# Optimization experiments

Hardware: AMD Instinct MI355X
Metric: run time of the kernel (lower is better)

Reference implementation:

```python
import jax, jax.numpy as jnp
import numpy as np

N_NODES = 100000
N_EDGES = 1600000
D = 128


def setup_inputs() -> dict:
    key = jax.random.key(0)
    k1, k2, k3, k4, k5 = jax.random.split(key, 5)
    x = jax.random.normal(k1, (N_NODES, D), dtype=jnp.float32)
    edge_index = jax.random.randint(k2, (2, N_EDGES), 0, N_NODES, dtype=jnp.int32)
    edge_weight = jax.random.uniform(k3, (N_EDGES,), dtype=jnp.float32)
    W_lin = jax.random.normal(k4, (D, D), dtype=jnp.float32) / np.sqrt(D)
    W_gcn = jax.random.normal(k5, (D, D), dtype=jnp.float32) / np.sqrt(D)
    return {"x": x, "edge_index": edge_index, "edge_weight": edge_weight,
            "W_lin": W_lin, "W_gcn": W_gcn}


def reference(x, edge_index, edge_weight, W_lin, W_gcn):
    # hl = Linear(x) (no bias)
    hl = x @ W_lin  # [N, D]

    # GCNConv with add_self_loops=False, normalize=True, no bias:
    row = edge_index[0]  # src
    col = edge_index[1]  # dst
    # symmetric gcn_norm from edge weights (degree scattered onto dst)
    deg = jax.ops.segment_sum(edge_weight, col, num_segments=x.shape[0])  # [N]
    deg_inv_sqrt = jnp.where(deg > 0, jax.lax.rsqrt(deg), 0.0)
    norm = deg_inv_sqrt[row] * edge_weight * deg_inv_sqrt[col]  # [E]

    h = x @ W_gcn  # [N, D] transform before propagate
    msg = h[row] * norm[:, None]  # [E, D] gather + scale
    hr = jax.ops.segment_sum(msg, col, num_segments=x.shape[0])  # scatter-add [N, D]

    return hl + hr
```

## Files before the change

kernel.cpp:

```cpp
#include <hip/hip_runtime.h>

#define NN 100000
#define NE 1600000
#define DD 128
#define NB 1563
#define HIST_BLKS 256
#define CAST_BLKS 752
#define WT2_BLKS  16
#define K1_BLKS (HIST_BLKS + CAST_BLKS + WT2_BLKS)
#define BINCAP 1536

typedef __attribute__((ext_vector_type(8))) short bf16x8;
typedef __attribute__((ext_vector_type(4))) float f32x4;

__device__ inline unsigned short f2bf(float f) {
  union { float f; unsigned u; } v; v.f = f;
  unsigned r = (v.u + 0x7FFF + ((v.u >> 16) & 1)) >> 16;
  return (unsigned short)r;
}

__global__ __launch_bounds__(512) void kb1(const int* __restrict__ col,
    const float* __restrict__ x, const float* __restrict__ Wl, const float* __restrict__ Wg,
    unsigned* __restrict__ hist, unsigned short* __restrict__ xb, unsigned short* __restrict__ WT2) {
  __shared__ unsigned h1[NB];
  int b = blockIdx.x, tid = threadIdx.x;
  if (b < HIST_BLKS) {
    for (int i = tid; i < NB; i += 512) h1[i] = 0;
    __syncthreads();
    for (int e = b * 512 + tid; e < NE; e += HIST_BLKS * 512)
      atomicAdd(&h1[((unsigned)col[e]) >> 6], 1u);
    __syncthreads();
    for (int i = tid; i < NB; i += 512) hist[(size_t)i * HIST_BLKS + b] = h1[i];
  } else if (b < HIST_BLKS + CAST_BLKS) {
    int bb = b - HIST_BLKS;
    const int total8 = NN * DD / 8;
    for (int i = bb * 512 + tid; i < total8; i += CAST_BLKS * 512) {
      float4 a = *(const float4*)&x[i * 8];
      float4 q = *(const float4*)&x[i * 8 + 4];
      unsigned short o[8] = {f2bf(a.x), f2bf(a.y), f2bf(a.z), f2bf(a.w),
                             f2bf(q.x), f2bf(q.y), f2bf(q.z), f2bf(q.w)};
      *(uint4*)&xb[i * 8] = *(uint4*)o;
    }
  } else {
    int bb = b - HIST_BLKS - CAST_BLKS;
    int j = bb * 8 + (tid >> 6);
    int l = tid & 63;
    for (int k = l; k < 256; k += 64) {
      const float* W = (k < DD) ? Wl : Wg;
      WT2[j * 256 + k] = f2bf(W[(k & (DD - 1)) * DD + j]);
    }
  }
}

__global__ __launch_bounds__(256) void kb2a(const unsigned* __restrict__ hist,
    unsigned* __restrict__ binTotal) {
  int w = (blockIdx.x * 256 + threadIdx.x) >> 6, l = threadIdx.x & 63;
  if (w >= NB) return;
  unsigned s = 0;
  for (int k = l; k < HIST_BLKS; k += 64) s += hist[(size_t)w * HIST_BLKS + k];
  #pragma unroll
  for (int off = 32; off >= 1; off >>= 1) s += __shfl_down(s, off, 64);
  if (l == 0) binTotal[w] = s;
}

__global__ __launch_bounds__(512) void kb2b(const unsigned* __restrict__ binTotal,
    unsigned* __restrict__ binBase) {
  __shared__ unsigned ps[512];
  int t = threadIdx.x;
  unsigned v[4], s = 0;
  #pragma unroll
  for (int k = 0; k < 4; k++) { int i = t * 4 + k; v[k] = (i < NB) ? binTotal[i] : 0; s += v[k]; }
  ps[t] = s;
  __syncthreads();
  for (int off = 1; off < 512; off <<= 1) {
    unsigned u = (t >= off) ? ps[t - off] : 0;
    __syncthreads();
    ps[t] += u;
    __syncthreads();
  }
  unsigned run = ps[t] - s;
  #pragma unroll
  for (int k = 0; k < 4; k++) { int i = t * 4 + k; if (i < NB + 1) binBase[i] = run; run += v[k]; }
}

__global__ __launch_bounds__(256) void kb2c(const unsigned* __restrict__ hist,
    const unsigned* __restrict__ binBase, unsigned* __restrict__ off) {
  int w = (blockIdx.x * 256 + threadIdx.x) >> 6, l = threadIdx.x & 63;
  if (w >= NB) return;
  unsigned v[4], s = 0;
  #pragma unroll
  for (int k = 0; k < 4; k++) { v[k] = hist[(size_t)w * HIST_BLKS + l * 4 + k]; s += v[k]; }
  unsigned incl = s;
  #pragma unroll
  for (int o = 1; o < 64; o <<= 1) { unsigned tt = __shfl_up(incl, o, 64); if (l >= o) incl += tt; }
  unsigned run = binBase[w] + incl - s;
  #pragma unroll
  for (int k = 0; k < 4; k++) { off[(size_t)(l * 4 + k) * NB + w] = run; run += v[k]; }
}

__global__ __launch_bounds__(512) void kb3(const int* __restrict__ row, const int* __restrict__ col,
    const float* __restrict__ ew, const unsigned* __restrict__ off,
    unsigned long long* __restrict__ entries) {
  __shared__ unsigned cnt[NB];
  int b = blockIdx.x, tid = threadIdx.x;
  for (int i = tid; i < NB; i += 512) cnt[i] = off[(size_t)b * NB + i];
  __syncthreads();
  for (int e = b * 512 + tid; e < NE; e += HIST_BLKS * 512) {
    int c = col[e];
    unsigned pos = atomicAdd(&cnt[((unsigned)c) >> 6], 1u);
    entries[pos] = ((unsigned long long)__float_as_uint(ew[e]) << 32)
                 | ((unsigned)row[e] << 6) | (unsigned)(c & 63);
  }
}

__global__ __launch_bounds__(256) void kb4(const unsigned long long* __restrict__ entries,
    const unsigned* __restrict__ binBase, float* __restrict__ dis) {
  __shared__ unsigned degFx[64];
  int bin = blockIdx.x, tid = threadIdx.x;
  if (tid < 64) degFx[tid] = 0;
  __syncthreads();
  unsigned s0 = binBase[bin], n = binBase[bin + 1] - s0;
  for (unsigned i = tid; i < n; i += 256) {
    unsigned long long e = entries[s0 + i];
    float w = __uint_as_float((unsigned)(e >> 32));
    atomicAdd(&degFx[(unsigned)e & 63], (unsigned)(w * 67108864.0f + 0.5f));
  }
  __syncthreads();
  if (tid < 64) {
    int node = bin * 64 + tid;
    if (node < NN) {
      float d = (float)degFx[tid] * (1.0f / 67108864.0f);
      dis[node] = (d > 0.0f) ? rsqrtf(d) : 0.0f;
    }
  }
}

__global__ __launch_bounds__(512) void kb5(const unsigned long long* __restrict__ entries,
    const unsigned* __restrict__ binBase, const float* __restrict__ dis,
    const unsigned short* __restrict__ xb, unsigned short* __restrict__ yb) {
  __shared__ unsigned long long raw[BINCAP], srt[BINCAP];
  __shared__ unsigned short rnk[BINCAP];
  __shared__ unsigned cnt64[64];
  __shared__ unsigned base64[64];
  int bin = blockIdx.x, tid = threadIdx.x;
  unsigned s0 = binBase[bin];
  int n = (int)(binBase[bin + 1] - s0);
  if (n > BINCAP) n = BINCAP;
  if (tid < 64) cnt64[tid] = 0;
  for (int i = tid; i < n; i += 512) raw[i] = entries[s0 + i];
  __syncthreads();
  for (int i = tid; i < n; i += 512)
    rnk[i] = (unsigned short)atomicAdd(&cnt64[(unsigned)raw[i] & 63], 1u);
  __syncthreads();
  if (tid < 64) {
    unsigned v = cnt64[tid], incl = v;
    #pragma unroll
    for (int o = 1; o < 64; o <<= 1) { unsigned t2 = __shfl_up(incl, o, 64); if (tid >= o) incl += t2; }
    base64[tid] = incl - v;
  }
  __syncthreads();
  for (int i = tid; i < n; i += 512) {
    unsigned long long e = raw[i];
    srt[base64[(unsigned)e & 63] + rnk[i]] = e;
  }
  __syncthreads();
  for (int i = tid; i < n; i += 512) {
    unsigned long long e = srt[i];
    unsigned src = ((unsigned)e) >> 6;
    float wn = __uint_as_float((unsigned)(e >> 32)) * dis[src];
    srt[i] = ((unsigned long long)__float_as_uint(wn) << 32) | (unsigned)(e & 0xFFFFFFFFu);
  }
  __syncthreads();
  int wv = tid >> 6, lane = tid & 63, grp = lane >> 4, l16 = lane & 15;
  for (int dd = 0; dd < 8; ++dd) {
    int d = wv * 8 + dd;
    int c = bin * 64 + d;
    if (c >= NN) break;
    int e0 = base64[d], m = cnt64[d];
    float acc[8] = {};
    for (int i = 0; i < m; i += 8) {
      int ja = i + grp, jb = i + 4 + grp;
      unsigned sa = 0, sb = 0;
      float wa = 0.f, wb = 0.f;
      if (ja < m) { unsigned long long e = srt[e0 + ja]; sa = ((unsigned)e) >> 6; wa = __uint_as_float((unsigned)(e >> 32)); }
      if (jb < m) { unsigned long long e = srt[e0 + jb]; sb = ((unsigned)e) >> 6; wb = __uint_as_float((unsigned)(e >> 32)); }
      uint4 ha = *(const uint4*)&xb[(size_t)sa * DD + l16 * 8];
      uint4 hb = *(const uint4*)&xb[(size_t)sb * DD + l16 * 8];
      union { uint4 v; unsigned u[4]; } qa, qb;
      qa.v = ha; qb.v = hb;
      #pragma unroll
      for (int k = 0; k < 4; k++) {
        union { unsigned u; float f; } lo, hi;
        lo.u = qa.u[k] << 16;
        hi.u = qa.u[k] & 0xFFFF0000u;
        acc[2 * k]     += wa * lo.f;
        acc[2 * k + 1] += wa * hi.f;
        lo.u = qb.u[k] << 16;
        hi.u = qb.u[k] & 0xFFFF0000u;
        acc[2 * k]     += wb * lo.f;
        acc[2 * k + 1] += wb * hi.f;
      }
    }
    #pragma unroll
    for (int k = 0; k < 8; k++) {
      acc[k] += __shfl_xor(acc[k], 16, 64);
      acc[k] += __shfl_xor(acc[k], 32, 64);
    }
    if (grp == 0) {
      float dc = dis[c];
      unsigned short o[8] = {f2bf(acc[0] * dc), f2bf(acc[1] * dc), f2bf(acc[2] * dc),
                             f2bf(acc[3] * dc), f2bf(acc[4] * dc), f2bf(acc[5] * dc),
                             f2bf(acc[6] * dc), f2bf(acc[7] * dc)};
      *(uint4*)&yb[(size_t)c * DD + l16 * 8] = *(uint4*)o;
    }
  }
}

__global__ __launch_bounds__(256) void k_gemm(const unsigned short* __restrict__ xb,
    const unsigned short* __restrict__ yb, const unsigned short* __restrict__ WT2,
    float* __restrict__ out, int N) {
  __shared__ __align__(16) unsigned short Bl[128 * 256];
  __shared__ __align__(16) unsigned short Al[64 * 256];
  int t = threadIdx.x;
  int rowbase = blockIdx.x * 64;

  const uint4* WTv = (const uint4*)WT2;
  #pragma unroll
  for (int i = 0; i < 16; i++) {
    int ci = t + i * 256;
    int j = ci >> 5, c16 = ci & 31;
    uint4 v = WTv[ci];
    int byte = j * 512 + c16 * 16;
    byte ^= (j & 7) << 4;
    *(uint4*)((char*)Bl + byte) = v;
  }
  #pragma unroll
  for (int i = 0; i < 8; i++) {
    int ci = t + i * 256;
    int r = ci >> 5, c16 = ci & 31;
    int gr = rowbase + r;
    uint4 v = make_uint4(0, 0, 0, 0);
    if (gr < N) {
      if (c16 < 16) v = *(const uint4*)&xb[(size_t)gr * DD + c16 * 8];
      else          v = *(const uint4*)&yb[(size_t)gr * DD + (c16 - 16) * 8];
    }
    int byte = r * 512 + c16 * 16;
    byte ^= (r & 7) << 4;
    *(uint4*)((char*)Al + byte) = v;
  }
  __syncthreads();

  int wid = t >> 6, lane = t & 63;
  int wn = wid * 32;
  int l15 = lane & 15, l4 = lane >> 4;
  f32x4 acc[4][2] = {};
  #pragma unroll
  for (int kk = 0; kk < 8; kk++) {
    bf16x8 af[4], bfr[2];
    #pragma unroll
    for (int m = 0; m < 4; m++) {
      int r = m * 16 + l15;
      int byte = r * 512 + kk * 64 + l4 * 16;
      byte ^= (r & 7) << 4;
      af[m] = *(const bf16x8*)((const char*)Al + byte);
    }
    #pragma unroll
    for (int n = 0; n < 2; n++) {
      int r = wn + n * 16 + l15;
      int byte = r * 512 + kk * 64 + l4 * 16;
      byte ^= (r & 7) << 4;
      bfr[n] = *(const bf16x8*)((const char*)Bl + byte);
    }
    #pragma unroll
    for (int m = 0; m < 4; m++)
      #pragma unroll
      for (int n = 0; n < 2; n++)
        acc[m][n] = __builtin_amdgcn_mfma_f32_16x16x32_bf16(af[m], bfr[n], acc[m][n], 0, 0, 0);
  }

  #pragma unroll
  for (int m = 0; m < 4; m++) {
    int gr0 = rowbase + m * 16 + l4 * 4;
    #pragma unroll
    for (int n = 0; n < 2; n++) {
      int gc = wn + n * 16 + l15;
      #pragma unroll
      for (int j = 0; j < 4; j++) {
        int gr = gr0 + j;
        if (gr < N) out[(size_t)gr * DD + gc] = acc[m][n][j];
      }
    }
  }
}

extern "C" void kernel_launch(void* const* d_in, const int* in_sizes, int n_in,
                              void* d_out, int out_size, void* d_ws, size_t ws_size,
                              hipStream_t stream) {
  const float* x  = (const float*)d_in[0];
  const int*   ei = (const int*)d_in[1];
  const float* ew = (const float*)d_in[2];
  const float* Wl = (const float*)d_in[3];
  const float* Wg = (const float*)d_in[4];
  float* out = (float*)d_out;
  const int* row = ei;
  const int* col = ei + NE;

  const size_t MB = 1u << 20;
  char* base = (char*)d_ws;
  unsigned* hist     = (unsigned*)(base);
  unsigned* off      = (unsigned*)(base + 2 * MB);
  unsigned* binTotal = (unsigned*)(base + 4 * MB);
  unsigned* binBase  = (unsigned*)(base + 4 * MB + 32768);
  unsigned long long* entries = (unsigned long long*)(base + 5 * MB);
  float* dis = (float*)(base + 18 * MB);
  unsigned short* xb = (unsigned short*)(base + 19 * MB);
  unsigned short* yb = (unsigned short*)(base + 45 * MB);
  unsigned short* WT2 = (unsigned short*)(base + 71 * MB);

  kb1<<<K1_BLKS, 512, 0, stream>>>(col, x, Wl, Wg, hist, xb, WT2);
  kb2a<<<(NB + 3) / 4, 256, 0, stream>>>(hist, binTotal);
  kb2b<<<1, 512, 0, stream>>>(binTotal, binBase);
  kb2c<<<(NB + 3) / 4, 256, 0, stream>>>(hist, binBase, off);
  kb3<<<HIST_BLKS, 512, 0, stream>>>(row, col, ew, off, entries);
  kb4<<<NB, 256, 0, stream>>>(entries, binBase, dis);
  kb5<<<NB, 512, 0, stream>>>(entries, binBase, dis, xb, yb);
  k_gemm<<<(NN + 63) / 64, 256, 0, stream>>>(xb, yb, WT2, out, NN);
}
```

Baseline: 161.2 us.

## Halve histogram blocks, unroll gather loop 4-way, use nontemporal output stores

Three separate changes. The histogram/scatter stage now uses 128 blocks instead of 256, which shrinks the per-block offset table and the scan work. The aggregation loop now issues four independent bf16 row gathers per iteration instead of two, so more memory loads are in flight. The GEMM output writes use nontemporal stores to avoid polluting cache. Fewer histogram blocks means less parallelism in the scatter kernel, and the deeper unroll raises register pressure.

```diff
diff --git a/kernel.cpp b/kernel.cpp
--- a/kernel.cpp
+++ b/kernel.cpp
@@ -4,7 +4,8 @@
 #define NE 1600000
 #define DD 128
 #define NB 1563
-#define HIST_BLKS 256
+#define HIST_BLKS 128
+#define PB (HIST_BLKS / 64)
 #define CAST_BLKS 752
 #define WT2_BLKS  16
 #define K1_BLKS (HIST_BLKS + CAST_BLKS + WT2_BLKS)
@@ -87,15 +88,15 @@
     const unsigned* __restrict__ binBase, unsigned* __restrict__ off) {
   int w = (blockIdx.x * 256 + threadIdx.x) >> 6, l = threadIdx.x & 63;
   if (w >= NB) return;
-  unsigned v[4], s = 0;
-  #pragma unroll
-  for (int k = 0; k < 4; k++) { v[k] = hist[(size_t)w * HIST_BLKS + l * 4 + k]; s += v[k]; }
+  unsigned v[PB], s = 0;
+  #pragma unroll
+  for (int k = 0; k < PB; k++) { v[k] = hist[(size_t)w * HIST_BLKS + l * PB + k]; s += v[k]; }
   unsigned incl = s;
   #pragma unroll
   for (int o = 1; o < 64; o <<= 1) { unsigned tt = __shfl_up(incl, o, 64); if (l >= o) incl += tt; }
   unsigned run = binBase[w] + incl - s;
   #pragma unroll
-  for (int k = 0; k < 4; k++) { off[(size_t)(l * 4 + k) * NB + w] = run; run += v[k]; }
+  for (int k = 0; k < PB; k++) { off[(size_t)(l * PB + k) * NB + w] = run; run += v[k]; }
 }
 
 __global__ __launch_bounds__(512) void kb3(const int* __restrict__ row, const int* __restrict__ col,
@@ -178,27 +179,31 @@
     if (c >= NN) break;
     int e0 = base64[d], m = cnt64[d];
     float acc[8] = {};
-    for (int i = 0; i < m; i += 8) {
-      int ja = i + grp, jb = i + 4 + grp;
-      unsigned sa = 0, sb = 0;
-      float wa = 0.f, wb = 0.f;
-      if (ja < m) { unsigned long long e = srt[e0 + ja]; sa = ((unsigned)e) >> 6; wa = __uint_as_float((unsigned)(e >> 32)); }
-      if (jb < m) { unsigned long long e = srt[e0 + jb]; sb = ((unsigned)e) >> 6; wb = __uint_as_float((unsigned)(e >> 32)); }
-      uint4 ha = *(const uint4*)&xb[(size_t)sa * DD + l16 * 8];
-      uint4 hb = *(const uint4*)&xb[(size_t)sb * DD + l16 * 8];
-      union { uint4 v; unsigned u[4]; } qa, qb;
-      qa.v = ha; qb.v = hb;
+    for (int i = 0; i < m; i += 16) {
+      int j0 = i + grp, j1 = i + 4 + grp, j2 = i + 8 + grp, j3 = i + 12 + grp;
+      unsigned sA = 0, sB = 0, sC = 0, sD = 0;
+      float wA = 0.f, wB = 0.f, wC = 0.f, wD = 0.f;
+      if (j0 < m) { unsigned long long e = srt[e0 + j0]; sA = ((unsigned)e) >> 6; wA = __uint_as_float((unsigned)(e >> 32)); }
+      if (j1 < m) { unsigned long long e = srt[e0 + j1]; sB = ((unsigned)e) >> 6; wB = __uint_as_float((unsigned)(e >> 32)); }
+      if (j2 < m) { unsigned long long e = srt[e0 + j2]; sC = ((unsigned)e) >> 6; wC = __uint_as_float((unsigned)(e >> 32)); }
+      if (j3 < m) { unsigned long long e = srt[e0 + j3]; sD = ((unsigned)e) >> 6; wD = __uint_as_float((unsigned)(e >> 32)); }
+      uint4 qA = *(const uint4*)&xb[(size_t)sA * DD + l16 * 8];
+      uint4 qB = *(const uint4*)&xb[(size_t)sB * DD + l16 * 8];
+      uint4 qC = *(const uint4*)&xb[(size_t)sC * DD + l16 * 8];
+      uint4 qD = *(const uint4*)&xb[(size_t)sD * DD + l16 * 8];
+      union { uint4 v; unsigned u[4]; } ua, ub, uc, ud;
+      ua.v = qA; ub.v = qB; uc.v = qC; ud.v = qD;
       #pragma unroll
       for (int k = 0; k < 4; k++) {
         union { unsigned u; float f; } lo, hi;
-        lo.u = qa.u[k] << 16;
-        hi.u = qa.u[k] & 0xFFFF0000u;
-        acc[2 * k]     += wa * lo.f;
-        acc[2 * k + 1] += wa * hi.f;
-        lo.u = qb.u[k] << 16;
-        hi.u = qb.u[k] & 0xFFFF0000u;
-        acc[2 * k]     += wb * lo.f;
-        acc[2 * k + 1] += wb * hi.f;
+        lo.u = ua.u[k] << 16;          hi.u = ua.u[k] & 0xFFFF0000u;
+        acc[2 * k] += wA * lo.f;       acc[2 * k + 1] += wA * hi.f;
+        lo.u = ub.u[k] << 16;          hi.u = ub.u[k] & 0xFFFF0000u;
+        acc[2 * k] += wB * lo.f;       acc[2 * k + 1] += wB * hi.f;
+        lo.u = uc.u[k] << 16;          hi.u = uc.u[k] & 0xFFFF0000u;
+        acc[2 * k] += wC * lo.f;       acc[2 * k + 1] += wC * hi.f;
+        lo.u = ud.u[k] << 16;          hi.u = ud.u[k] & 0xFFFF0000u;
+        acc[2 * k] += wD * lo.f;       acc[2 * k + 1] += wD * hi.f;
       }
     }
     #pragma unroll
@@ -287,7 +292,7 @@
       #pragma unroll
       for (int j = 0; j < 4; j++) {
         int gr = gr0 + j;
-        if (gr < N) out[(size_t)gr * DD + gc] = acc[m][n][j];
+        if (gr < N) __builtin_nontemporal_store(acc[m][n][j], &out[(size_t)gr * DD + gc]);
       }
     }
   }
```

New measurement: 171.3 us. +6.3%, slower.
